# Kernel tuning notes

Hardware: AMD Instinct MI355X
Metric: run time of the kernel (lower is better)

The kernel has to match this reference:

```python
import jax, jax.numpy as jnp
import numpy as np

HEADS = 16
DIM_HEAD = 64
LN_EPS = 1e-5
COS_EPS = 1e-8


def setup_inputs() -> dict:
    key = jax.random.key(0)
    ks = jax.random.split(key, 5)
    dim = 1024
    inner = HEADS * DIM_HEAD
    q = jax.random.normal(ks[0], (4, 1024, dim), dtype=jnp.float32)
    k = jax.random.normal(ks[1], (4, 2048, dim), dtype=jnp.float32)
    v = jax.random.normal(ks[2], (4, 2048, dim), dtype=jnp.float32)
    W_in = jax.random.normal(ks[3], (dim, inner), dtype=jnp.float32) * (1.0 / np.sqrt(dim))
    W_out = jax.random.normal(ks[4], (inner, dim), dtype=jnp.float32) * (1.0 / np.sqrt(inner))
    ln_gamma = jnp.ones((dim,), dtype=jnp.float32)
    ln_beta = jnp.zeros((dim,), dtype=jnp.float32)
    b_out = jnp.zeros((dim,), dtype=jnp.float32)
    return {"q": q, "k": k, "v": v, "ln_gamma": ln_gamma, "ln_beta": ln_beta,
            "W_in": W_in, "W_out": W_out, "b_out": b_out}


def _layernorm(x, gamma, beta):
    mu = jnp.mean(x, axis=-1, keepdims=True)
    var = jnp.mean(jnp.square(x - mu), axis=-1, keepdims=True)  # biased, as torch
    return (x - mu) * jax.lax.rsqrt(var + LN_EPS) * gamma + beta


def _project(t, gamma, beta, W_in):
    # LayerNorm -> Linear(no bias) -> split heads: b n (h d) -> b h n d
    x = _layernorm(t, gamma, beta) @ W_in
    b, n, _ = x.shape
    return x.reshape(b, n, HEADS, DIM_HEAD).transpose(0, 2, 1, 3)


def reference(q, k, v, ln_gamma, ln_beta, W_in, W_out, b_out):
    f_q = _project(q, ln_gamma, ln_beta, W_in)  # [b,h,n,d]
    f_k = _project(k, ln_gamma, ln_beta, W_in)  # [b,h,m,d]
    f_v = _project(v, ln_gamma, ln_beta, W_in)  # [b,h,m,d]
    dots = jnp.einsum('bhnd,bhmd->bhnm', f_q, f_k)
    qn = jnp.linalg.norm(f_q, axis=-1, keepdims=True)          # [b,h,n,1]
    kn = jnp.linalg.norm(f_k, axis=-1, keepdims=True)          # [b,h,m,1]
    attn = dots / (qn * kn.transpose(0, 1, 3, 2) + COS_EPS)    # [b,h,n,m]
    out = jnp.einsum('bhnm,bhmd->bhnd', attn, f_v)             # [b,h,n,d]
    b, h, n, d = out.shape
    out = out.transpose(0, 2, 1, 3).reshape(b, n, h * d)       # b n (h d)
    return out @ W_out + b_out
```

## Files before the change

### kernel.cpp

```cpp
#include <hip/hip_runtime.h>

constexpr int BATCH = 4;
constexpr int SEQQ  = 1024;
constexpr int SEQK  = 2048;
constexpr int DIM   = 1024;
constexpr int NH    = 16;
constexpr int DH    = 64;
constexpr int RQ    = BATCH * SEQQ;
constexpr int RK    = BATCH * SEQK;
constexpr int RTOT  = RQ + 2 * RK;
constexpr int BH    = BATCH * NH;
constexpr float LN_EPS = 1e-5f;

typedef _Float16 f16;
typedef __attribute__((ext_vector_type(8))) _Float16 f16x8;
typedef __attribute__((ext_vector_type(4))) float f32x4;

__device__ __forceinline__ void async16(const void* g, void* l) {
  __builtin_amdgcn_global_load_lds(
      (const __attribute__((address_space(1))) void*)g,
      (__attribute__((address_space(3))) void*)l, 16, 0, 0);
}

__global__ void __launch_bounds__(256) ln_to_f16(
    const float* __restrict__ q, const float* __restrict__ k,
    const float* __restrict__ v, const float* __restrict__ gamma,
    const float* __restrict__ beta, f16* __restrict__ a_h) {
  int row = blockIdx.x;
  const float* src;
  if (row < RQ)            src = q + (size_t)row * DIM;
  else if (row < RQ + RK)  src = k + (size_t)(row - RQ) * DIM;
  else                     src = v + (size_t)(row - RQ - RK) * DIM;
  int t = threadIdx.x;
  float4 x = ((const float4*)src)[t];
  float s  = x.x + x.y + x.z + x.w;
  float s2 = x.x * x.x + x.y * x.y + x.z * x.z + x.w * x.w;
  for (int off = 32; off; off >>= 1) {
    s  += __shfl_down(s, off);
    s2 += __shfl_down(s2, off);
  }
  __shared__ float ls[4], ls2[4];
  __shared__ float smu, srs;
  int wid = t >> 6;
  if ((t & 63) == 0) { ls[wid] = s; ls2[wid] = s2; }
  __syncthreads();
  if (t == 0) {
    float S1 = ls[0] + ls[1] + ls[2] + ls[3];
    float S2 = ls2[0] + ls2[1] + ls2[2] + ls2[3];
    float mu  = S1 / DIM;
    float var = S2 / DIM - mu * mu;
    smu = mu;
    srs = rsqrtf(var + LN_EPS);
  }
  __syncthreads();
  float mu = smu, rs = srs;
  float4 g = ((const float4*)gamma)[t];
  float4 b = ((const float4*)beta)[t];
  union { f16 h[4]; uint2 u; } o;
  o.h[0] = (f16)((x.x - mu) * rs * g.x + b.x);
  o.h[1] = (f16)((x.y - mu) * rs * g.y + b.y);
  o.h[2] = (f16)((x.z - mu) * rs * g.z + b.z);
  o.h[3] = (f16)((x.w - mu) * rs * g.w + b.w);
  ((uint2*)(a_h + (size_t)row * DIM))[t] = o.u;
}

__global__ void __launch_bounds__(256) transpose_f16(
    const float* __restrict__ W0, const float* __restrict__ W1,
    f16* __restrict__ T0, f16* __restrict__ T1) {
  const float* W = blockIdx.z ? W1 : W0;
  f16* T = blockIdx.z ? T1 : T0;
  __shared__ float tile[32][33];
  int tx = threadIdx.x & 31, ty = threadIdx.x >> 5;
  int k0 = blockIdx.x * 32, n0 = blockIdx.y * 32;
#pragma unroll
  for (int i = 0; i < 4; i++)
    tile[ty + 8 * i][tx] = W[(size_t)(k0 + ty + 8 * i) * DIM + n0 + tx];
  __syncthreads();
#pragma unroll
  for (int i = 0; i < 4; i++)
    T[(size_t)(n0 + ty + 8 * i) * DIM + k0 + tx] = (f16)tile[tx][ty + 8 * i];
}

template <bool OUT_F16, bool NORMS, bool BIAS>
__global__ void __launch_bounds__(256) mfma_gemm(
    const f16* __restrict__ A, const f16* __restrict__ Bt,
    void* __restrict__ Cout, const float* __restrict__ bias,
    float* __restrict__ rq, float* __restrict__ rk) {
  __shared__ f16 As[2][128 * 32];
  __shared__ f16 Bs[2][128 * 32];
  const int t = threadIdx.x;
  const int wid = t >> 6;
  const int lane = t & 63;
  const int row0 = blockIdx.x * 128;
  const int col0 = blockIdx.y * 128;
  const int wm = (wid >> 1) * 64;
  const int wn = (wid & 1) * 64;

  const f16* gA = A + (size_t)(row0 + 32 * wid + (lane >> 2)) * DIM + (lane & 3) * 8;
  const f16* gB = Bt + (size_t)(col0 + 32 * wid + (lane >> 2)) * DIM + (lane & 3) * 8;
  f16* lA0 = As[0] + 32 * wid * 32;
  f16* lA1 = As[1] + 32 * wid * 32;
  f16* lB0 = Bs[0] + 32 * wid * 32;
  f16* lB1 = Bs[1] + 32 * wid * 32;

  f32x4 acc[4][4];
#pragma unroll
  for (int i = 0; i < 4; i++)
#pragma unroll
    for (int j = 0; j < 4; j++) acc[i][j] = (f32x4){0.f, 0.f, 0.f, 0.f};

  const int mrow = lane & 15;
  const int kq   = (lane >> 4) * 8;

  for (int kt = 0; kt < DIM / 64; ++kt) {
    if (kt) __syncthreads();
    const int ko = kt * 64;
    async16(gA + ko,                lA0);
    async16(gA + ko + 16 * DIM,     lA0 + 512);
    async16(gB + ko,                lB0);
    async16(gB + ko + 16 * DIM,     lB0 + 512);
    async16(gA + ko + 32,           lA1);
    async16(gA + ko + 32 + 16 * DIM, lA1 + 512);
    async16(gB + ko + 32,           lB1);
    async16(gB + ko + 32 + 16 * DIM, lB1 + 512);
    __syncthreads();

#pragma unroll
    for (int h = 0; h < 2; ++h) {
      f16x8 af[4], bf[4];
#pragma unroll
      for (int i = 0; i < 4; i++)
        af[i] = *(const f16x8*)(As[h] + (wm + i * 16 + mrow) * 32 + kq);
#pragma unroll
      for (int j = 0; j < 4; j++)
        bf[j] = *(const f16x8*)(Bs[h] + (wn + j * 16 + mrow) * 32 + kq);
#pragma unroll
      for (int i = 0; i < 4; i++)
#pragma unroll
        for (int j = 0; j < 4; j++)
          acc[i][j] = __builtin_amdgcn_mfma_f32_16x16x32_f16(af[i], bf[j], acc[i][j], 0, 0, 0);
    }
  }

  const int ccol = lane & 15;
  const int crow = (lane >> 4) * 4;
  if (OUT_F16) {
    f16* C = (f16*)Cout;
#pragma unroll
    for (int j = 0; j < 4; j++) {
      const int col = col0 + wn + j * 16 + ccol;
#pragma unroll
      for (int i = 0; i < 4; i++) {
        f16* Cp = C + (size_t)(row0 + wm + i * 16 + crow) * DIM + col;
#pragma unroll
        for (int r = 0; r < 4; r++) Cp[(size_t)r * DIM] = (f16)acc[i][j][r];
      }
    }
  } else {
    float* C = (float*)Cout;
#pragma unroll
    for (int j = 0; j < 4; j++) {
      const int col = col0 + wn + j * 16 + ccol;
      float bv = BIAS ? bias[col] : 0.f;
#pragma unroll
      for (int i = 0; i < 4; i++) {
        float* Cp = C + (size_t)(row0 + wm + i * 16 + crow) * DIM + col;
#pragma unroll
        for (int r = 0; r < 4; r++) Cp[(size_t)r * DIM] = acc[i][j][r] + bv;
      }
    }
  }

  if (NORMS) {
    float sums[4][4];
#pragma unroll
    for (int i = 0; i < 4; i++)
#pragma unroll
      for (int r = 0; r < 4; r++) {
        float s = 0.f;
#pragma unroll
        for (int j = 0; j < 4; j++) s += acc[i][j][r] * acc[i][j][r];
        sums[i][r] = s;
      }
#pragma unroll
    for (int off = 1; off < 16; off <<= 1)
#pragma unroll
      for (int i = 0; i < 4; i++)
#pragma unroll
        for (int r = 0; r < 4; r++)
          sums[i][r] += __shfl_xor(sums[i][r], off);
    if ((lane & 15) == 0) {
      const int head = (col0 + wn) >> 6;
#pragma unroll
      for (int i = 0; i < 4; i++)
#pragma unroll
        for (int r = 0; r < 4; r++) {
          const int row = row0 + wm + i * 16 + crow + r;
          const float inv = rsqrtf(sums[i][r]);
          if (row < RQ)            rq[(size_t)row * NH + head] = inv;
          else if (row < RQ + RK)  rk[(size_t)(row - RQ) * NH + head] = inv;
        }
    }
  }
}

__global__ void __launch_bounds__(256) s_kernel(
    const f16* __restrict__ f, const float* __restrict__ rk,
    float* __restrict__ S4) {
  const int bh = blockIdx.x;
  const int b = bh >> 4, h = bh & 15;
  const int mbase = blockIdx.y * 512;
  const int t = threadIdx.x;
  __shared__ float ks[32][68];
  __shared__ float vs[32][68];
  const int lm   = t >> 3;
  const int lseg = (t & 7) * 8;
  const int d1 = (t & 15) * 4;
  const int d2 = (t >> 4) * 4;
  float acc[4][4] = {{0.f}};
  const f16* fk_base = f + ((size_t)RQ + (size_t)b * SEQK) * DIM + h * DH;
  const f16* fv_base = f + ((size_t)RQ + RK + (size_t)b * SEQK) * DIM + h * DH;

  for (int sub = 0; sub < 16; ++sub) {
    const int m = mbase + sub * 32 + lm;
    const float scale = rk[(size_t)(b * SEQK + m) * NH + h];
    f16x8 kv = *(const f16x8*)(fk_base + (size_t)m * DIM + lseg);
    f16x8 vv = *(const f16x8*)(fv_base + (size_t)m * DIM + lseg);
    __syncthreads();
#pragma unroll
    for (int e = 0; e < 8; e++) {
      ks[lm][lseg + e] = (float)kv[e] * scale;
      vs[lm][lseg + e] = (float)vv[e];
    }
    __syncthreads();
#pragma unroll
    for (int mm = 0; mm < 32; ++mm) {
      float4 kk = *(const float4*)&ks[mm][d1];
      float4 vv2 = *(const float4*)&vs[mm][d2];
      acc[0][0] = fmaf(kk.x, vv2.x, acc[0][0]);
      acc[0][1] = fmaf(kk.x, vv2.y, acc[0][1]);
      acc[0][2] = fmaf(kk.x, vv2.z, acc[0][2]);
      acc[0][3] = fmaf(kk.x, vv2.w, acc[0][3]);
      acc[1][0] = fmaf(kk.y, vv2.x, acc[1][0]);
      acc[1][1] = fmaf(kk.y, vv2.y, acc[1][1]);
      acc[1][2] = fmaf(kk.y, vv2.z, acc[1][2]);
      acc[1][3] = fmaf(kk.y, vv2.w, acc[1][3]);
      acc[2][0] = fmaf(kk.z, vv2.x, acc[2][0]);
      acc[2][1] = fmaf(kk.z, vv2.y, acc[2][1]);
      acc[2][2] = fmaf(kk.z, vv2.z, acc[2][2]);
      acc[2][3] = fmaf(kk.z, vv2.w, acc[2][3]);
      acc[3][0] = fmaf(kk.w, vv2.x, acc[3][0]);
      acc[3][1] = fmaf(kk.w, vv2.y, acc[3][1]);
      acc[3][2] = fmaf(kk.w, vv2.z, acc[3][2]);
      acc[3][3] = fmaf(kk.w, vv2.w, acc[3][3]);
    }
  }
  float* Sp = S4 + ((size_t)blockIdx.y * BH + bh) * DH * DH;
#pragma unroll
  for (int i = 0; i < 4; i++)
#pragma unroll
    for (int j = 0; j < 4; j++)
      Sp[(d1 + i) * DH + (d2 + j)] = acc[i][j];
}

__global__ void __launch_bounds__(256) outhead_kernel(
    const f16* __restrict__ f, const float* __restrict__ S4,
    const float* __restrict__ rq, f16* __restrict__ ao) {
  const int bh = blockIdx.x;
  const int b = bh >> 4, h = bh & 15;
  const int nbase = blockIdx.y * 64;
  const int t = threadIdx.x;
  __shared__ float Sl[64][68];
  __shared__ float Ql[64][68];
  {
    const int r = t >> 2;
    const int seg = (t & 3) * 16;
    const float* Sp = S4 + (size_t)bh * DH * DH + r * DH + seg;
    constexpr size_t STR = (size_t)BH * DH * DH;
#pragma unroll
    for (int c = 0; c < 4; c++) {
      float4 s0 = ((const float4*)Sp)[c];
      float4 s1 = ((const float4*)(Sp + STR))[c];
      float4 s2 = ((const float4*)(Sp + 2 * STR))[c];
      float4 s3 = ((const float4*)(Sp + 3 * STR))[c];
      float4 s;
      s.x = s0.x + s1.x + s2.x + s3.x;
      s.y = s0.y + s1.y + s2.y + s3.y;
      s.z = s0.z + s1.z + s2.z + s3.z;
      s.w = s0.w + s1.w + s2.w + s3.w;
      *(float4*)&Sl[r][seg + 4 * c] = s;
    }
    const f16* Qp = f + ((size_t)b * SEQQ + nbase + r) * DIM + h * DH + seg;
    f16x8 q0 = *(const f16x8*)Qp;
    f16x8 q1 = *(const f16x8*)(Qp + 8);
#pragma unroll
    for (int e = 0; e < 8; e++) {
      Ql[r][seg + e]     = (float)q0[e];
      Ql[r][seg + 8 + e] = (float)q1[e];
    }
  }
  __syncthreads();
  const int d2 = (t & 15) * 4;
  const int g  = t >> 4;
#pragma unroll
  for (int i = 0; i < 4; ++i) {
    const int n = i * 16 + g;
    float4 acc = {0.f, 0.f, 0.f, 0.f};
#pragma unroll 8
    for (int d1 = 0; d1 < 64; ++d1) {
      float qv = Ql[n][d1];
      float4 sv = *(const float4*)&Sl[d1][d2];
      acc.x = fmaf(qv, sv.x, acc.x);
      acc.y = fmaf(qv, sv.y, acc.y);
      acc.z = fmaf(qv, sv.z, acc.z);
      acc.w = fmaf(qv, sv.w, acc.w);
    }
    const float r = rq[((size_t)b * SEQQ + nbase + n) * NH + h];
    union { f16 h4[4]; uint2 u; } o;
    o.h4[0] = (f16)(acc.x * r);
    o.h4[1] = (f16)(acc.y * r);
    o.h4[2] = (f16)(acc.z * r);
    o.h4[3] = (f16)(acc.w * r);
    *(uint2*)(ao + ((size_t)b * SEQQ + nbase + n) * DIM + h * DH + d2) = o.u;
  }
}

extern "C" void kernel_launch(void* const* d_in, const int* in_sizes, int n_in,
                              void* d_out, int out_size, void* d_ws, size_t ws_size,
                              hipStream_t stream) {
  const float* q     = (const float*)d_in[0];
  const float* k     = (const float*)d_in[1];
  const float* v     = (const float*)d_in[2];
  const float* gamma = (const float*)d_in[3];
  const float* beta  = (const float*)d_in[4];
  const float* W_in  = (const float*)d_in[5];
  const float* W_out = (const float*)d_in[6];
  const float* b_out = (const float*)d_in[7];
  float* out = (float*)d_out;

  char* w = (char*)d_ws;
  f16*   f      = (f16*)w;
  f16*   a_h    = f + (size_t)RTOT * DIM;
  f16*   wt_in  = a_h + (size_t)RTOT * DIM;
  f16*   wt_out = wt_in + (size_t)DIM * DIM;
  float* rqb    = (float*)(wt_out + (size_t)DIM * DIM);
  float* rkb    = rqb + (size_t)RQ * NH;
  float* S4     = rkb + (size_t)RK * NH;
  f16*   ao     = a_h;

  ln_to_f16<<<RTOT, 256, 0, stream>>>(q, k, v, gamma, beta, a_h);
  transpose_f16<<<dim3(DIM / 32, DIM / 32, 2), 256, 0, stream>>>(
      W_in, W_out, wt_in, wt_out);

  mfma_gemm<true, true, false><<<dim3(RTOT / 128, DIM / 128), 256, 0, stream>>>(
      a_h, wt_in, f, nullptr, rqb, rkb);

  s_kernel<<<dim3(BH, 4), 256, 0, stream>>>(f, rkb, S4);

  outhead_kernel<<<dim3(BH, SEQQ / 64), 256, 0, stream>>>(f, S4, rqb, ao);

  mfma_gemm<false, false, true><<<dim3(RQ / 128, DIM / 128), 256, 0, stream>>>(
      ao, wt_out, out, b_out, nullptr, nullptr);
}
```

Before: 257.3 us.

## Retune LN, GEMM swizzle and tiles, and S-kernel split with prefetch

LayerNorm now handles one row per wavefront, reducing with xor shuffles and no shared-memory barriers. The GEMM gets an XOR-style swizzle on its LDS k-chunks to cut bank conflicts, plus a 64-row tile variant that gives the small output projection more blocks. The K^T V kernel splits the sequence into 8 slices instead of 4 and register-prefetches the next sub-tile, which raises parallelism. The cost is more partial sums for outhead to reduce, and smaller tiles reuse each B tile less.

```diff
diff --git a/kernel.cpp b/kernel.cpp
--- a/kernel.cpp
+++ b/kernel.cpp
@@ -10,6 +10,7 @@
 constexpr int RK    = BATCH * SEQK;
 constexpr int RTOT  = RQ + 2 * RK;
 constexpr int BH    = BATCH * NH;
+constexpr int NSLC  = 8;
 constexpr float LN_EPS = 1e-5f;
 
 typedef _Float16 f16;
@@ -26,42 +27,38 @@
     const float* __restrict__ q, const float* __restrict__ k,
     const float* __restrict__ v, const float* __restrict__ gamma,
     const float* __restrict__ beta, f16* __restrict__ a_h) {
-  int row = blockIdx.x;
+  const int row = blockIdx.x * 4 + (threadIdx.x >> 6);
+  const int lane = threadIdx.x & 63;
   const float* src;
   if (row < RQ)            src = q + (size_t)row * DIM;
   else if (row < RQ + RK)  src = k + (size_t)(row - RQ) * DIM;
   else                     src = v + (size_t)(row - RQ - RK) * DIM;
-  int t = threadIdx.x;
-  float4 x = ((const float4*)src)[t];
-  float s  = x.x + x.y + x.z + x.w;
-  float s2 = x.x * x.x + x.y * x.y + x.z * x.z + x.w * x.w;
-  for (int off = 32; off; off >>= 1) {
-    s  += __shfl_down(s, off);
-    s2 += __shfl_down(s2, off);
-  }
-  __shared__ float ls[4], ls2[4];
-  __shared__ float smu, srs;
-  int wid = t >> 6;
-  if ((t & 63) == 0) { ls[wid] = s; ls2[wid] = s2; }
-  __syncthreads();
-  if (t == 0) {
-    float S1 = ls[0] + ls[1] + ls[2] + ls[3];
-    float S2 = ls2[0] + ls2[1] + ls2[2] + ls2[3];
-    float mu  = S1 / DIM;
-    float var = S2 / DIM - mu * mu;
-    smu = mu;
-    srs = rsqrtf(var + LN_EPS);
-  }
-  __syncthreads();
-  float mu = smu, rs = srs;
-  float4 g = ((const float4*)gamma)[t];
-  float4 b = ((const float4*)beta)[t];
-  union { f16 h[4]; uint2 u; } o;
-  o.h[0] = (f16)((x.x - mu) * rs * g.x + b.x);
-  o.h[1] = (f16)((x.y - mu) * rs * g.y + b.y);
-  o.h[2] = (f16)((x.z - mu) * rs * g.z + b.z);
-  o.h[3] = (f16)((x.w - mu) * rs * g.w + b.w);
-  ((uint2*)(a_h + (size_t)row * DIM))[t] = o.u;
+  float4 x[4];
+  float s = 0.f, s2 = 0.f;
+#pragma unroll
+  for (int c = 0; c < 4; c++) {
+    x[c] = ((const float4*)src)[c * 64 + lane];
+    s  += x[c].x + x[c].y + x[c].z + x[c].w;
+    s2 += x[c].x * x[c].x + x[c].y * x[c].y + x[c].z * x[c].z + x[c].w * x[c].w;
+  }
+#pragma unroll
+  for (int off = 1; off < 64; off <<= 1) {
+    s  += __shfl_xor(s, off);
+    s2 += __shfl_xor(s2, off);
+  }
+  const float mu = s / DIM;
+  const float rs = rsqrtf(s2 / DIM - mu * mu + LN_EPS);
+#pragma unroll
+  for (int c = 0; c < 4; c++) {
+    float4 g = ((const float4*)gamma)[c * 64 + lane];
+    float4 b = ((const float4*)beta)[c * 64 + lane];
+    union { f16 h[4]; uint2 u; } o;
+    o.h[0] = (f16)((x[c].x - mu) * rs * g.x + b.x);
+    o.h[1] = (f16)((x[c].y - mu) * rs * g.y + b.y);
+    o.h[2] = (f16)((x[c].z - mu) * rs * g.z + b.z);
+    o.h[3] = (f16)((x[c].w - mu) * rs * g.w + b.w);
+    ((uint2*)(a_h + (size_t)row * DIM))[c * 64 + lane] = o.u;
+  }
 }
 
 __global__ void __launch_bounds__(256) transpose_f16(
@@ -81,63 +78,68 @@
     T[(size_t)(n0 + ty + 8 * i) * DIM + k0 + tx] = (f16)tile[tx][ty + 8 * i];
 }
 
-template <bool OUT_F16, bool NORMS, bool BIAS>
+template <int MT, bool OUT_F16, bool NORMS, bool BIAS>
 __global__ void __launch_bounds__(256) mfma_gemm(
     const f16* __restrict__ A, const f16* __restrict__ Bt,
     void* __restrict__ Cout, const float* __restrict__ bias,
     float* __restrict__ rq, float* __restrict__ rk) {
-  __shared__ f16 As[2][128 * 32];
+  constexpr int JT = (MT == 128) ? 4 : 2;
+  __shared__ f16 As[2][MT * 32];
   __shared__ f16 Bs[2][128 * 32];
   const int t = threadIdx.x;
   const int wid = t >> 6;
   const int lane = t & 63;
-  const int row0 = blockIdx.x * 128;
+  const int row0 = blockIdx.x * MT;
   const int col0 = blockIdx.y * 128;
-  const int wm = (wid >> 1) * 64;
-  const int wn = (wid & 1) * 64;
-
-  const f16* gA = A + (size_t)(row0 + 32 * wid + (lane >> 2)) * DIM + (lane & 3) * 8;
-  const f16* gB = Bt + (size_t)(col0 + 32 * wid + (lane >> 2)) * DIM + (lane & 3) * 8;
-  f16* lA0 = As[0] + 32 * wid * 32;
-  f16* lA1 = As[1] + 32 * wid * 32;
+  const int wm = (MT == 128) ? (wid >> 1) * 64 : 0;
+  const int wn = (MT == 128) ? (wid & 1) * 64 : wid * 32;
+
+  const int rB = 32 * wid + (lane >> 2);
+  const int qB = ((lane & 3) - ((rB >> 1) & 3)) & 3;
+  const f16* gB = Bt + (size_t)(col0 + rB) * DIM + qB * 8;
   f16* lB0 = Bs[0] + 32 * wid * 32;
   f16* lB1 = Bs[1] + 32 * wid * 32;
-
-  f32x4 acc[4][4];
+  const int rA = (MT == 128 ? 32 : 16) * wid + (lane >> 2);
+  const int qA = ((lane & 3) - ((rA >> 1) & 3)) & 3;
+  const f16* gA = A + (size_t)(row0 + rA) * DIM + qA * 8;
+  f16* lA0 = As[0] + (MT == 128 ? 32 : 16) * wid * 32;
+  f16* lA1 = As[1] + (MT == 128 ? 32 : 16) * wid * 32;
+
+  f32x4 acc[4][JT];
 #pragma unroll
   for (int i = 0; i < 4; i++)
 #pragma unroll
-    for (int j = 0; j < 4; j++) acc[i][j] = (f32x4){0.f, 0.f, 0.f, 0.f};
+    for (int j = 0; j < JT; j++) acc[i][j] = (f32x4){0.f, 0.f, 0.f, 0.f};
 
   const int mrow = lane & 15;
-  const int kq   = (lane >> 4) * 8;
+  const int kq_p = (((lane >> 4) + ((lane >> 1) & 3)) & 3) * 8;
 
   for (int kt = 0; kt < DIM / 64; ++kt) {
     if (kt) __syncthreads();
     const int ko = kt * 64;
-    async16(gA + ko,                lA0);
-    async16(gA + ko + 16 * DIM,     lA0 + 512);
-    async16(gB + ko,                lB0);
-    async16(gB + ko + 16 * DIM,     lB0 + 512);
-    async16(gA + ko + 32,           lA1);
-    async16(gA + ko + 32 + 16 * DIM, lA1 + 512);
-    async16(gB + ko + 32,           lB1);
+    async16(gA + ko,      lA0);
+    if (MT == 128) async16(gA + ko + 16 * DIM, lA0 + 512);
+    async16(gB + ko,      lB0);
+    async16(gB + ko + 16 * DIM, lB0 + 512);
+    async16(gA + ko + 32, lA1);
+    if (MT == 128) async16(gA + ko + 32 + 16 * DIM, lA1 + 512);
+    async16(gB + ko + 32, lB1);
     async16(gB + ko + 32 + 16 * DIM, lB1 + 512);
     __syncthreads();
 
 #pragma unroll
     for (int h = 0; h < 2; ++h) {
-      f16x8 af[4], bf[4];
+      f16x8 af[4], bf[JT];
 #pragma unroll
       for (int i = 0; i < 4; i++)
-        af[i] = *(const f16x8*)(As[h] + (wm + i * 16 + mrow) * 32 + kq);
-#pragma unroll
-      for (int j = 0; j < 4; j++)
-        bf[j] = *(const f16x8*)(Bs[h] + (wn + j * 16 + mrow) * 32 + kq);
+        af[i] = *(const f16x8*)(As[h] + (wm + i * 16 + mrow) * 32 + kq_p);
+#pragma unroll
+      for (int j = 0; j < JT; j++)
+        bf[j] = *(const f16x8*)(Bs[h] + (wn + j * 16 + mrow) * 32 + kq_p);
 #pragma unroll
       for (int i = 0; i < 4; i++)
 #pragma unroll
-        for (int j = 0; j < 4; j++)
+        for (int j = 0; j < JT; j++)
           acc[i][j] = __builtin_amdgcn_mfma_f32_16x16x32_f16(af[i], bf[j], acc[i][j], 0, 0, 0);
     }
   }
@@ -147,7 +149,7 @@
   if (OUT_F16) {
     f16* C = (f16*)Cout;
 #pragma unroll
-    for (int j = 0; j < 4; j++) {
+    for (int j = 0; j < JT; j++) {
       const int col = col0 + wn + j * 16 + ccol;
 #pragma unroll
       for (int i = 0; i < 4; i++) {
@@ -159,7 +161,7 @@
   } else {
     float* C = (float*)Cout;
 #pragma unroll
-    for (int j = 0; j < 4; j++) {
+    for (int j = 0; j < JT; j++) {
       const int col = col0 + wn + j * 16 + ccol;
       float bv = BIAS ? bias[col] : 0.f;
 #pragma unroll
@@ -171,7 +173,7 @@
     }
   }
 
-  if (NORMS) {
+  if (NORMS && MT == 128) {
     float sums[4][4];
 #pragma unroll
     for (int i = 0; i < 4; i++)
@@ -179,7 +181,7 @@
       for (int r = 0; r < 4; r++) {
         float s = 0.f;
 #pragma unroll
-        for (int j = 0; j < 4; j++) s += acc[i][j][r] * acc[i][j][r];
+        for (int j = 0; j < JT; j++) s += acc[i][j][r] * acc[i][j][r];
         sums[i][r] = s;
       }
 #pragma unroll
@@ -209,7 +211,7 @@
     float* __restrict__ S4) {
   const int bh = blockIdx.x;
   const int b = bh >> 4, h = bh & 15;
-  const int mbase = blockIdx.y * 512;
+  const int mbase = blockIdx.y * (SEQK / NSLC);
   const int t = threadIdx.x;
   __shared__ float ks[32][68];
   __shared__ float vs[32][68];
@@ -221,18 +223,26 @@
   const f16* fk_base = f + ((size_t)RQ + (size_t)b * SEQK) * DIM + h * DH;
   const f16* fv_base = f + ((size_t)RQ + RK + (size_t)b * SEQK) * DIM + h * DH;
 
-  for (int sub = 0; sub < 16; ++sub) {
-    const int m = mbase + sub * 32 + lm;
-    const float scale = rk[(size_t)(b * SEQK + m) * NH + h];
-    f16x8 kv = *(const f16x8*)(fk_base + (size_t)m * DIM + lseg);
-    f16x8 vv = *(const f16x8*)(fv_base + (size_t)m * DIM + lseg);
+  int m = mbase + lm;
+  f16x8 kv = *(const f16x8*)(fk_base + (size_t)m * DIM + lseg);
+  f16x8 vv = *(const f16x8*)(fv_base + (size_t)m * DIM + lseg);
+  float sc = rk[(size_t)(b * SEQK + m) * NH + h];
+
+  constexpr int SUBS = SEQK / NSLC / 32;
+  for (int sub = 0; sub < SUBS; ++sub) {
     __syncthreads();
 #pragma unroll
     for (int e = 0; e < 8; e++) {
-      ks[lm][lseg + e] = (float)kv[e] * scale;
+      ks[lm][lseg + e] = (float)kv[e] * sc;
       vs[lm][lseg + e] = (float)vv[e];
     }
     __syncthreads();
+    if (sub + 1 < SUBS) {
+      m = mbase + (sub + 1) * 32 + lm;
+      kv = *(const f16x8*)(fk_base + (size_t)m * DIM + lseg);
+      vv = *(const f16x8*)(fv_base + (size_t)m * DIM + lseg);
+      sc = rk[(size_t)(b * SEQK + m) * NH + h];
+    }
 #pragma unroll
     for (int mm = 0; mm < 32; ++mm) {
       float4 kk = *(const float4*)&ks[mm][d1];
@@ -279,15 +289,12 @@
     constexpr size_t STR = (size_t)BH * DH * DH;
 #pragma unroll
     for (int c = 0; c < 4; c++) {
-      float4 s0 = ((const float4*)Sp)[c];
-      float4 s1 = ((const float4*)(Sp + STR))[c];
-      float4 s2 = ((const float4*)(Sp + 2 * STR))[c];
-      float4 s3 = ((const float4*)(Sp + 3 * STR))[c];
-      float4 s;
-      s.x = s0.x + s1.x + s2.x + s3.x;
-      s.y = s0.y + s1.y + s2.y + s3.y;
-      s.z = s0.z + s1.z + s2.z + s3.z;
-      s.w = s0.w + s1.w + s2.w + s3.w;
+      float4 s = {0.f, 0.f, 0.f, 0.f};
+#pragma unroll
+      for (int p = 0; p < NSLC; p++) {
+        float4 sp = ((const float4*)(Sp + p * STR))[c];
+        s.x += sp.x; s.y += sp.y; s.z += sp.z; s.w += sp.w;
+      }
       *(float4*)&Sl[r][seg + 4 * c] = s;
     }
     const f16* Qp = f + ((size_t)b * SEQQ + nbase + r) * DIM + h * DH + seg;
@@ -348,17 +355,17 @@
   float* S4     = rkb + (size_t)RK * NH;
   f16*   ao     = a_h;
 
-  ln_to_f16<<<RTOT, 256, 0, stream>>>(q, k, v, gamma, beta, a_h);
+  ln_to_f16<<<RTOT / 4, 256, 0, stream>>>(q, k, v, gamma, beta, a_h);
   transpose_f16<<<dim3(DIM / 32, DIM / 32, 2), 256, 0, stream>>>(
       W_in, W_out, wt_in, wt_out);
 
-  mfma_gemm<true, true, false><<<dim3(RTOT / 128, DIM / 128), 256, 0, stream>>>(
+  mfma_gemm<128, true, true, false><<<dim3(RTOT / 128, DIM / 128), 256, 0, stream>>>(
       a_h, wt_in, f, nullptr, rqb, rkb);
 
-  s_kernel<<<dim3(BH, 4), 256, 0, stream>>>(f, rkb, S4);
+  s_kernel<<<dim3(BH, NSLC), 256, 0, stream>>>(f, rkb, S4);
 
   outhead_kernel<<<dim3(BH, SEQQ / 64), 256, 0, stream>>>(f, S4, rqb, ao);
 
-  mfma_gemm<false, false, true><<<dim3(RQ / 128, DIM / 128), 256, 0, stream>>>(
+  mfma_gemm<64, false, false, true><<<dim3(RQ / 64, DIM / 128), 256, 0, stream>>>(
       ao, wt_out, out, b_out, nullptr, nullptr);
 }
```

Measured after the change: 244.5 us. -5.0%, faster.
